# Performance work log

Measured on AMD Instinct MI355X. Metric: run time of the kernel, lower is better.

## Reference

```python
import jax, jax.numpy as jnp
import numpy as np

EMBED = 768
HEADS = 12
HEAD_DIM = EMBED // HEADS
NUM_BUCKETS = 32
MAX_DISTANCE = 128


def _relative_buckets(tgt_len, src_len):
    ctx = jnp.arange(tgt_len)[:, None]
    mem = jnp.arange(src_len)[None, :]
    rel = mem - ctx                                  # [T, S]
    nb = NUM_BUCKETS // 2                            # 16
    buckets = (rel > 0).astype(jnp.int32) * nb
    rp = jnp.abs(rel)
    max_exact = nb // 2                              # 8
    is_small = rp < max_exact
    rp_safe = jnp.maximum(rp, 1).astype(jnp.float32)
    large = max_exact + (
        jnp.log(rp_safe / max_exact) / np.log(MAX_DISTANCE / max_exact) * (nb - max_exact)
    ).astype(jnp.int32)
    large = jnp.minimum(large, nb - 1)
    buckets = buckets + jnp.where(is_small, rp, large)
    return buckets                                   # [T, S] int32


def setup_inputs() -> dict:
    key = jax.random.key(0)
    ks = jax.random.split(key, 12)
    T, B, E = 2048, 2, EMBED
    def xavier(k, shape, gain=1.0):
        fan_in, fan_out = shape[0], shape[1]
        a = gain * np.sqrt(6.0 / (fan_in + fan_out))
        return jax.random.uniform(k, shape, jnp.float32, -a, a)
    g = 1.0 / np.sqrt(2.0)
    return {
        "query": jax.random.normal(ks[0], (T, B, E), jnp.float32),
        "key": jax.random.normal(ks[1], (T, B, E), jnp.float32),
        "value": jax.random.normal(ks[2], (T, B, E), jnp.float32),
        "key_padding_mask": jnp.zeros((B, T), dtype=bool),
        # weights stored [in, out] (transpose of torch Linear)
        "Wq": xavier(ks[3], (E, E), g), "bq": jnp.zeros((E,), jnp.float32),
        "Wk": xavier(ks[4], (E, E), g), "bk": jnp.zeros((E,), jnp.float32),
        "Wv": xavier(ks[5], (E, E), g), "bv": jnp.zeros((E,), jnp.float32),
        "Wo": xavier(ks[6], (E, E), 1.0), "bo": jnp.zeros((E,), jnp.float32),
        "rel_bias": jax.random.normal(ks[7], (NUM_BUCKETS, HEADS), jnp.float32)
        * np.sqrt(2.0 / (NUM_BUCKETS + HEADS)),
    }


def reference(query, key, value, key_padding_mask, Wq, bq, Wk, bk, Wv, bv, Wo, bo, rel_bias):
    T, B, E = query.shape
    S = key.shape[0]
    scaling = HEAD_DIM ** -0.5
    q = (query @ Wq + bq) * scaling
    k = key @ Wk + bk
    v = value @ Wv + bv
    # [T,B,E] -> [B,H,T,D]
    def split_heads(x, L):
        return x.reshape(L, B, HEADS, HEAD_DIM).transpose(1, 2, 0, 3)
    qh, kh, vh = split_heads(q, T), split_heads(k, S), split_heads(v, S)
    # T5 relative position bias: [H, T, S]
    buckets = _relative_buckets(T, S)
    position_bias = rel_bias[buckets].transpose(2, 0, 1)  # [H,T,S]
    scores = jnp.einsum("bhtd,bhsd->bhts", qh, kh) + position_bias[None]
    scores = jnp.where(key_padding_mask[:, None, None, :], -jnp.inf, scores)
    probs = jax.nn.softmax(scores, axis=-1)
    attn = jnp.einsum("bhts,bhsd->bhtd", probs, vh)
    attn = attn.transpose(2, 0, 1, 3).reshape(T, B, E)
    return attn @ Wo + bo
```

## Files before the change

### kernel.cpp

```cpp
#include <hip/hip_runtime.h>
#include <hip/hip_bf16.h>

typedef __bf16 bf16;
typedef __bf16 bf16x8 __attribute__((ext_vector_type(8)));
typedef float f32x4 __attribute__((ext_vector_type(4)));

#define EMB 768
#define NH 12
#define HD 64
#define SEQ 2048
#define NBATCH 2
#define NREL (2 * SEQ - 1)
#define LOG2E 1.44269504088896f

__device__ __forceinline__ int swz(int bo) { return bo ^ ((bo >> 3) & 0x70); }
__device__ __forceinline__ int swz256(int bo) { return bo ^ ((bo >> 4) & 0x70); }
__device__ __forceinline__ int kpos(int s) {
  return (s & 0x23) | ((s & 0x04) << 2) | ((s & 0x18) >> 1);
}
__device__ __forceinline__ float fexp2(float x) {
  return __builtin_amdgcn_exp2f(x);
}

typedef __attribute__((address_space(3))) unsigned int lds_u32;
typedef __attribute__((address_space(1))) unsigned int glb_u32;
__device__ __forceinline__ void gld16(const void* g, void* l) {
  __builtin_amdgcn_global_load_lds((const glb_u32*)g, (lds_u32*)l, 16, 0, 0);
}

__global__ __launch_bounds__(256) void k_setup(
    const float* __restrict__ Xq, const float* __restrict__ Xk,
    const float* __restrict__ Xv, const float* __restrict__ Wq,
    const float* __restrict__ Wk, const float* __restrict__ Wv,
    const float* __restrict__ Wo, const unsigned char* __restrict__ mask,
    const float* __restrict__ rel_bias, bf16* __restrict__ ximg,
    bf16* __restrict__ wimg, float* __restrict__ bias_tab,
    unsigned long long* __restrict__ mbits) {
  __shared__ __align__(16) bf16 T[64 * 128];
  const int idx = blockIdx.x;
  const int tid = threadIdx.x;
  if (idx < 1152) {
    const int z = idx / 384, rem = idx % 384;
    const int mb = rem % 32, ks = rem / 32;
    const float* X = z == 0 ? Xq : z == 1 ? Xk : Xv;
    const int m0 = mb * 128, k0 = ks * 64;
    char* img = (char*)ximg + ((size_t)(z * 32 + mb) * 12 + ks) * 16384;
#pragma unroll
    for (int it = 0; it < 4; ++it) {
      int i = tid + it * 256;
      int mr = i >> 3, kc8 = (i & 7) * 8;
      const float* xp = X + (size_t)(m0 + mr) * EMB + k0 + kc8;
      float4 f0 = *(const float4*)xp, f1 = *(const float4*)(xp + 4);
      bf16x8 hh;
      hh[0] = (bf16)f0.x; hh[1] = (bf16)f0.y; hh[2] = (bf16)f0.z; hh[3] = (bf16)f0.w;
      hh[4] = (bf16)f1.x; hh[5] = (bf16)f1.y; hh[6] = (bf16)f1.z; hh[7] = (bf16)f1.w;
      *(bf16x8*)(img + swz(mr * 128 + kc8 * 2)) = hh;
    }
  } else if (idx < 1440) {
    const int i = idx - 1152;
    const int z = i / 72, rem = i % 72;
    const int nb = rem % 6, ks = rem / 6;
    const float* W = z == 0 ? Wq : z == 1 ? Wk : z == 2 ? Wv : Wo;
    const int n0 = nb * 128, k0 = ks * 64;
    {
      int kk = tid >> 2, nn0 = (tid & 3) * 32;
      const float* wp = W + (size_t)(k0 + kk) * EMB + n0 + nn0;
#pragma unroll
      for (int jq = 0; jq < 4; ++jq) {
        float4 f0 = *(const float4*)(wp + jq * 8);
        float4 f1 = *(const float4*)(wp + jq * 8 + 4);
        bf16x8 hh;
        hh[0] = (bf16)f0.x; hh[1] = (bf16)f0.y; hh[2] = (bf16)f0.z; hh[3] = (bf16)f0.w;
        hh[4] = (bf16)f1.x; hh[5] = (bf16)f1.y; hh[6] = (bf16)f1.z; hh[7] = (bf16)f1.w;
        *(bf16x8*)((char*)T + swz256(kk * 256 + (nn0 + jq * 8) * 2)) = hh;
      }
    }
    __syncthreads();
    {
      int nr = tid >> 1, kh = tid & 1;
      char* img = (char*)wimg + ((size_t)(z * 6 + nb) * 12 + ks) * 16384;
#pragma unroll
      for (int jq = 0; jq < 4; ++jq) {
        union { bf16 e[8]; uint4 u; } pk;
#pragma unroll
        for (int q = 0; q < 8; ++q)
          pk.e[q] = *(const bf16*)((char*)T + swz256((kh * 32 + jq * 8 + q) * 256 + nr * 2));
        *(uint4*)(img + swz(nr * 128 + (kh * 32 + jq * 8) * 2)) = pk.u;
      }
    }
  } else if (idx < 1456) {
    int i = (idx - 1440) * 256 + tid;
    if (i < NREL) {
      int rel = i - (SEQ - 1);
      int bkt = (rel > 0) ? 16 : 0;
      int rp = rel < 0 ? -rel : rel;
      if (rp < 8) {
        bkt += rp;
      } else {
        float lf = (logf((float)rp * 0.125f) / 2.7725887222397811f) * 8.0f;
        int large = 8 + (int)lf;
        bkt += (large < 15) ? large : 15;
      }
      for (int h = 0; h < NH; ++h)
        bias_tab[h * NREL + i] = rel_bias[bkt * NH + h] * LOG2E;
    }
  } else {
    int wid = (idx - 1456) * 4 + (tid >> 6);
    int lane = tid & 63;
    int b = wid >> 5, wd = wid & 31;
    unsigned long long m = __ballot(mask[b * SEQ + wd * 64 + lane] != 0);
    if (lane == 0) mbits[wid] = m;
  }
}

__global__ __launch_bounds__(256) void k_proj_qkv(
    const bf16* __restrict__ ximg, const bf16* __restrict__ wimg,
    const float* __restrict__ bq, const float* __restrict__ bk,
    const float* __restrict__ bv, bf16* __restrict__ oq,
    bf16* __restrict__ gk, bf16* __restrict__ gv) {
  __shared__ __align__(16) bf16 AB[2][2][8192];
  const int z = blockIdx.z;
  const float* bias = z == 0 ? bq : z == 1 ? bk : bv;
  const float scale = z == 0 ? 0.125f * LOG2E : 1.0f;
  const int mb = blockIdx.x, nb = blockIdx.y;
  const int m0 = mb * 128, n0 = nb * 128;
  const int tid = threadIdx.x, lane = tid & 63, w = tid >> 6;
  const int c = lane & 15, g = lane >> 4;
  const int mo = (w >> 1) * 64, no = (w & 1) * 64;
  const char* abase = (const char*)ximg + (size_t)(z * 32 + mb) * 12 * 16384;
  const char* bbase = (const char*)wimg + (size_t)(z * 6 + nb) * 12 * 16384;

#define PISSUE(KS, BUF) do {                                               \
    const char* a_ = abase + (size_t)(KS) * 16384;                         \
    const char* b_ = bbase + (size_t)(KS) * 16384;                         \
    _Pragma("unroll") for (int ch = 0; ch < 4; ++ch) {                     \
      int ck = w * 4 + ch;                                                 \
      gld16(a_ + ck * 1024 + lane * 16, (char*)AB[BUF][0] + ck * 1024);    \
      gld16(b_ + ck * 1024 + lane * 16, (char*)AB[BUF][1] + ck * 1024);    \
    }                                                                      \
  } while (0)

  PISSUE(0, 0);
  f32x4 acc[4][4] = {};
  asm volatile("s_waitcnt vmcnt(0)" ::: "memory");
  __syncthreads();
  for (int ks = 0; ks < 12; ++ks) {
    const int cur = ks & 1;
    if (ks < 11) PISSUE(ks + 1, cur ^ 1);
    const char* As = (const char*)AB[cur][0];
    const char* Bs = (const char*)AB[cur][1];
    __builtin_amdgcn_s_setprio(1);
#pragma unroll
    for (int kk = 0; kk < 2; ++kk) {
      bf16x8 av[4], bvf[4];
#pragma unroll
      for (int mf = 0; mf < 4; ++mf)
        av[mf] = *(const bf16x8*)(As + swz((mo + mf * 16 + c) * 128 + kk * 64 + g * 16));
#pragma unroll
      for (int nf = 0; nf < 4; ++nf)
        bvf[nf] = *(const bf16x8*)(Bs + swz((no + nf * 16 + c) * 128 + kk * 64 + g * 16));
#pragma unroll
      for (int mf = 0; mf < 4; ++mf)
#pragma unroll
        for (int nf = 0; nf < 4; ++nf)
          acc[mf][nf] = __builtin_amdgcn_mfma_f32_16x16x32_bf16(bvf[nf], av[mf], acc[mf][nf], 0, 0, 0);
    }
    __builtin_amdgcn_s_setprio(0);
    if (ks < 11) {
      asm volatile("s_waitcnt vmcnt(0)" ::: "memory");
      __syncthreads();
    }
  }
#pragma unroll
  for (int nf = 0; nf < 4; ++nf) {
    int n = n0 + no + nf * 16 + g * 4;
    float4 b4 = *(const float4*)&bias[n];
#pragma unroll
    for (int mf = 0; mf < 4; ++mf) {
      int m = m0 + mo + mf * 16 + c;
      float v0 = (acc[mf][nf][0] + b4.x) * scale;
      float v1 = (acc[mf][nf][1] + b4.y) * scale;
      float v2 = (acc[mf][nf][2] + b4.z) * scale;
      float v3 = (acc[mf][nf][3] + b4.w) * scale;
      if (z == 0) {
        union { bf16 e[4]; uint2 u; } pk;
        pk.e[0] = (bf16)v0; pk.e[1] = (bf16)v1; pk.e[2] = (bf16)v2; pk.e[3] = (bf16)v3;
        *(uint2*)(oq + (size_t)m * EMB + n) = pk.u;
      } else if (z == 1) {
        int t = m >> 1, bb = m & 1;
        int hh = n >> 6, d = n & 63;
        union { bf16 e[4]; uint2 u; } pk;
        pk.e[0] = (bf16)v0; pk.e[1] = (bf16)v1; pk.e[2] = (bf16)v2; pk.e[3] = (bf16)v3;
        char* base = (char*)gk + ((size_t)(bb * NH + hh) * 32 + (t >> 6)) * 8192;
        *(uint2*)(base + swz(kpos(t & 63) * 128 + (d & ~7) * 2) + (d & 4) * 2) = pk.u;
      } else {
        int s = m >> 1, bb = m & 1;
        int hh = n >> 6, d0 = n & 63;
        char* base = (char*)gv + ((size_t)(bb * NH + hh) * 32 + (s >> 6)) * 8192;
        int sc2 = (s & 63) * 2;
        *(bf16*)(base + (((d0 + 0) * 128 + sc2) ^ (((d0 + 0) & 7) << 4))) = (bf16)v0;
        *(bf16*)(base + (((d0 + 1) * 128 + sc2) ^ (((d0 + 1) & 7) << 4))) = (bf16)v1;
        *(bf16*)(base + (((d0 + 2) * 128 + sc2) ^ (((d0 + 2) & 7) << 4))) = (bf16)v2;
        *(bf16*)(base + (((d0 + 3) * 128 + sc2) ^ (((d0 + 3) & 7) << 4))) = (bf16)v3;
      }
    }
  }
#undef PISSUE
}

__global__ __launch_bounds__(256) void k_proj_out(
    const bf16* __restrict__ aimg, const bf16* __restrict__ wimg,
    const float* __restrict__ bias, float* __restrict__ out) {
  __shared__ __align__(16) bf16 AB[2][2][8192];
  const int mb = blockIdx.x, nb = blockIdx.y;
  const int m0 = mb * 128, n0 = nb * 128;
  const int tid = threadIdx.x, lane = tid & 63, w = tid >> 6;
  const int c = lane & 15, g = lane >> 4;
  const int mo = (w >> 1) * 64, no = (w & 1) * 64;
  const char* abase = (const char*)aimg + (size_t)mb * 12 * 16384;
  const char* bbase = (const char*)wimg + (size_t)(3 * 6 + nb) * 12 * 16384;

#define PISSUE(KS, BUF) do {                                               \
    const char* a_ = abase + (size_t)(KS) * 16384;                         \
    const char* b_ = bbase + (size_t)(KS) * 16384;                         \
    _Pragma("unroll") for (int ch = 0; ch < 4; ++ch) {                     \
      int ck = w * 4 + ch;                                                 \
      gld16(a_ + ck * 1024 + lane * 16, (char*)AB[BUF][0] + ck * 1024);    \
      gld16(b_ + ck * 1024 + lane * 16, (char*)AB[BUF][1] + ck * 1024);    \
    }                                                                      \
  } while (0)

  PISSUE(0, 0);
  f32x4 acc[4][4] = {};
  asm volatile("s_waitcnt vmcnt(0)" ::: "memory");
  __syncthreads();
  for (int ks = 0; ks < 12; ++ks) {
    const int cur = ks & 1;
    if (ks < 11) PISSUE(ks + 1, cur ^ 1);
    const char* As = (const char*)AB[cur][0];
    const char* Bs = (const char*)AB[cur][1];
    __builtin_amdgcn_s_setprio(1);
#pragma unroll
    for (int kk = 0; kk < 2; ++kk) {
      bf16x8 av[4], bvf[4];
#pragma unroll
      for (int mf = 0; mf < 4; ++mf)
        av[mf] = *(const bf16x8*)(As + swz((mo + mf * 16 + c) * 128 + kk * 64 + g * 16));
#pragma unroll
      for (int nf = 0; nf < 4; ++nf)
        bvf[nf] = *(const bf16x8*)(Bs + swz((no + nf * 16 + c) * 128 + kk * 64 + g * 16));
#pragma unroll
      for (int mf = 0; mf < 4; ++mf)
#pragma unroll
        for (int nf = 0; nf < 4; ++nf)
          acc[mf][nf] = __builtin_amdgcn_mfma_f32_16x16x32_bf16(bvf[nf], av[mf], acc[mf][nf], 0, 0, 0);
    }
    __builtin_amdgcn_s_setprio(0);
    if (ks < 11) {
      asm volatile("s_waitcnt vmcnt(0)" ::: "memory");
      __syncthreads();
    }
  }
#pragma unroll
  for (int nf = 0; nf < 4; ++nf) {
    int n = n0 + no + nf * 16 + g * 4;
    float4 b4 = *(const float4*)&bias[n];
#pragma unroll
    for (int mf = 0; mf < 4; ++mf) {
      int m = m0 + mo + mf * 16 + c;
      float4 v;
      v.x = acc[mf][nf][0] + b4.x;
      v.y = acc[mf][nf][1] + b4.y;
      v.z = acc[mf][nf][2] + b4.z;
      v.w = acc[mf][nf][3] + b4.w;
      *(float4*)(out + (size_t)m * EMB + n) = v;
    }
  }
#undef PISSUE
}

__global__ __launch_bounds__(256, 4) void k_attn(
    const bf16* __restrict__ qb, const bf16* __restrict__ gk,
    const bf16* __restrict__ gv, const unsigned long long* __restrict__ mbits,
    const float* __restrict__ bias_tab, bf16* __restrict__ aimg) {
  __shared__ __align__(16) bf16 KV[2][2][4096];
  __shared__ float Bslow[384];
  const int bh = blockIdx.x;
  const int b = bh / NH, h = bh % NH;
  const int t0 = blockIdx.y * 64;
  const int tid = threadIdx.x;
  const int lane = tid & 63, w = tid >> 6;
  const int c = lane & 15, g = lane >> 4;
  const float NEGINF = -__builtin_inff();
  const int tl = w * 16 + c;

  const char* kimg = (const char*)gk + (size_t)bh * 32 * 8192;
  const char* vimg = (const char*)gv + (size_t)bh * 32 * 8192;

#define ISSUE(IT, BUF) do {                                                  \
    const char* ks_ = kimg + (size_t)(IT) * 8192;                            \
    const char* vs_ = vimg + (size_t)(IT) * 8192;                            \
    _Pragma("unroll") for (int jj = 0; jj < 2; ++jj) {                       \
      int ch = w * 2 + jj;                                                   \
      gld16(ks_ + ch * 1024 + lane * 16, (char*)KV[BUF][0] + ch * 1024);     \
      gld16(vs_ + ch * 1024 + lane * 16, (char*)KV[BUF][1] + ch * 1024);     \
    }                                                                        \
  } while (0)

  ISSUE(0, 0);
  bf16x8 qf[2];
  {
    const bf16* qp = qb + (size_t)((t0 + tl) * NBATCH + b) * EMB + h * 64 + g * 8;
    qf[0] = *(const bf16x8*)qp;
    qf[1] = *(const bf16x8*)(qp + 32);
  }
  const float* btab = bias_tab + h * NREL + (SEQ - 1);
  for (int j = tid; j < 384; j += 256) Bslow[j] = btab[j - 192];
  const float cpos = btab[SEQ - 1];
  const float cneg = btab[-(SEQ - 1)];

  bf16x8 ones8;
#pragma unroll
  for (int j = 0; j < 8; ++j) ones8[j] = (bf16)1.0f;

  float m_p = -1e30f;
  f32x4 lacc = {0.f, 0.f, 0.f, 0.f};
  f32x4 o[4] = {};

  asm volatile("s_waitcnt vmcnt(0)" ::: "memory");
  __syncthreads();

  for (int it = 0; it < 32; ++it) {
    const int cur = it & 1;
    if (it < 31) ISSUE(it + 1, cur ^ 1);
    const unsigned long long mb = mbits[b * 32 + it];
    const char* Ks = (const char*)KV[cur][0];
    const char* Vs = (const char*)KV[cur][1];

    f32x4 sacc[4] = {};
    __builtin_amdgcn_s_setprio(1);
#pragma unroll
    for (int kk = 0; kk < 2; ++kk) {
#pragma unroll
      for (int nf = 0; nf < 4; ++nf) {
        bf16x8 kf = *(const bf16x8*)(Ks + swz((nf * 16 + c) * 128 + kk * 64 + g * 16));
        sacc[nf] = __builtin_amdgcn_mfma_f32_16x16x32_bf16(kf, qf[kk], sacc[nf], 0, 0, 0);
      }
    }
    __builtin_amdgcn_s_setprio(0);

    const int s0 = it * 64;
    const int d = s0 - t0;
    const bool slow = (d > -192) && (d < 192);
    const float cb = slow ? 0.f : (d >= 192 ? cpos : cneg);

    if (slow) {
      const int bidx = d - tl + 192;
#pragma unroll
      for (int nf = 0; nf < 4; ++nf) {
        int sb = 32 * (nf >> 1) + g * 8 + (nf & 1) * 4;
#pragma unroll
        for (int r = 0; r < 4; ++r) sacc[nf][r] += Bslow[bidx + sb + r];
      }
    }
    if (mb) {
#pragma unroll
      for (int nf = 0; nf < 4; ++nf) {
        int sb = 32 * (nf >> 1) + g * 8 + (nf & 1) * 4;
#pragma unroll
        for (int r = 0; r < 4; ++r)
          if ((mb >> (sb + r)) & 1) sacc[nf][r] = NEGINF;
      }
    }
    f32x4 mx;
#pragma unroll
    for (int r = 0; r < 4; ++r)
      mx[r] = fmaxf(fmaxf(sacc[0][r], sacc[1][r]), fmaxf(sacc[2][r], sacc[3][r]));
    float rmax = fmaxf(fmaxf(mx[0], mx[1]), fmaxf(mx[2], mx[3]));
    rmax = fmaxf(rmax, __shfl_xor(rmax, 16, 64));
    rmax = fmaxf(rmax, __shfl_xor(rmax, 32, 64));
    const float rm = rmax + cb;

    if (!__all(rm <= m_p + 11.5f)) {
      float m_new = fmaxf(m_p, rm);
      float scl = fexp2(m_p - m_new);
      m_p = m_new;
#pragma unroll
      for (int r = 0; r < 4; ++r) {
        float so = __shfl(scl, g * 4 + r, 64);
        lacc[r] *= so;
#pragma unroll
        for (int nf2 = 0; nf2 < 4; ++nf2) o[nf2][r] *= so;
      }
    }
    const float msh = m_p - cb;
    bf16x8 pa[2];
#pragma unroll
    for (int kk = 0; kk < 2; ++kk)
#pragma unroll
      for (int j = 0; j < 8; ++j)
        pa[kk][j] = (bf16)fexp2(sacc[2 * kk + (j >> 2)][j & 3] - msh);

    __builtin_amdgcn_s_setprio(1);
    lacc = __builtin_amdgcn_mfma_f32_16x16x32_bf16(pa[0], ones8, lacc, 0, 0, 0);
    lacc = __builtin_amdgcn_mfma_f32_16x16x32_bf16(pa[1], ones8, lacc, 0, 0, 0);
#pragma unroll
    for (int kk = 0; kk < 2; ++kk) {
#pragma unroll
      for (int nf2 = 0; nf2 < 4; ++nf2) {
        bf16x8 vbf = *(const bf16x8*)(Vs + swz((nf2 * 16 + c) * 128 + kk * 64 + g * 16));
        o[nf2] = __builtin_amdgcn_mfma_f32_16x16x32_bf16(pa[kk], vbf, o[nf2], 0, 0, 0);
      }
    }
    __builtin_amdgcn_s_setprio(0);

    if (it < 31) {
      asm volatile("s_waitcnt vmcnt(0)" ::: "memory");
      __syncthreads();
    }
  }
#pragma unroll
  for (int r = 0; r < 4; ++r) {
    float inv = 1.0f / lacc[r];
    int t = t0 + w * 16 + g * 4 + r;
    int m = t * NBATCH + b;
    char* base = (char*)aimg + ((size_t)(m >> 7) * 12 + h) * 16384;
    int mr128 = (m & 127) * 128;
#pragma unroll
    for (int nf2 = 0; nf2 < 4; ++nf2) {
      int dd = nf2 * 16 + c;
      *(bf16*)(base + swz(mr128 + dd * 2)) = (bf16)(o[nf2][r] * inv);
    }
  }
#undef ISSUE
}

extern "C" void kernel_launch(void* const* d_in, const int* in_sizes, int n_in,
                              void* d_out, int out_size, void* d_ws, size_t ws_size,
                              hipStream_t stream) {
  const float* query = (const float*)d_in[0];
  const float* key_ = (const float*)d_in[1];
  const float* value = (const float*)d_in[2];
  const unsigned char* kpm = (const unsigned char*)d_in[3];
  const float* Wq = (const float*)d_in[4];
  const float* bq = (const float*)d_in[5];
  const float* Wk = (const float*)d_in[6];
  const float* bk = (const float*)d_in[7];
  const float* Wv = (const float*)d_in[8];
  const float* bv = (const float*)d_in[9];
  const float* Wo = (const float*)d_in[10];
  const float* bo = (const float*)d_in[11];
  const float* rel_bias = (const float*)d_in[12];
  float* out = (float*)d_out;

  char* ws = (char*)d_ws;
  const size_t SZb = (size_t)SEQ * NBATCH * EMB * sizeof(bf16);
  const size_t WIMG = (size_t)4 * 6 * 12 * 16384;
  bf16* qbb = (bf16*)(ws);
  bf16* gkb = (bf16*)(ws + SZb);
  bf16* gvb = (bf16*)(ws + 2 * SZb);
  bf16* wimg = (bf16*)(ws + 3 * SZb);
  float* bias_tab = (float*)(ws + 3 * SZb + WIMG);
  unsigned long long* mbits =
      (unsigned long long*)(ws + 3 * SZb + WIMG + 196608);
  bf16* ximg = (bf16*)(ws + 3 * SZb + WIMG + 196608 + 512);
  bf16* aimg = ximg;

  k_setup<<<1472, 256, 0, stream>>>(query, key_, value, Wq, Wk, Wv, Wo,
                                    kpm, rel_bias, ximg, wimg, bias_tab, mbits);
  k_proj_qkv<<<dim3(32, 6, 3), 256, 0, stream>>>(
      ximg, wimg, bq, bk, bv, qbb, gkb, gvb);
  k_attn<<<dim3(NBATCH * NH, SEQ / 64), 256, 0, stream>>>(
      qbb, gkb, gvb, mbits, bias_tab, aimg);
  k_proj_out<<<dim3(32, 6), 256, 0, stream>>>(aimg, wimg, bo, out);
}
```

Baseline: 94.32 us.

## Switch attention to 32x32x16 MFMA with split-KV waves and LDS merge

Rewrites the attention inner loop to use 32x32x16 bf16 MFMAs. Each pair of waves shares 32 query rows and splits the 64-key tile between them, with a final LDS-based merge of max, sum and partial outputs. The row sum is now accumulated in VALU instead of through ones-vector MFMAs, and P is re-laid out with permlane32 swaps for the PV MFMA. The K layout permutation in setup is dropped to match the new access pattern. This adds an epilogue merge with extra syncs and LDS traffic.

Result: slower. 114.8 us (+21.7%).

```diff
diff --git a/kernel.cpp b/kernel.cpp
--- a/kernel.cpp
+++ b/kernel.cpp
@@ -4,6 +4,7 @@
 typedef __bf16 bf16;
 typedef __bf16 bf16x8 __attribute__((ext_vector_type(8)));
 typedef float f32x4 __attribute__((ext_vector_type(4)));
+typedef float f32x16 __attribute__((ext_vector_type(16)));
 
 #define EMB 768
 #define NH 12
@@ -15,9 +16,6 @@
 
 __device__ __forceinline__ int swz(int bo) { return bo ^ ((bo >> 3) & 0x70); }
 __device__ __forceinline__ int swz256(int bo) { return bo ^ ((bo >> 4) & 0x70); }
-__device__ __forceinline__ int kpos(int s) {
-  return (s & 0x23) | ((s & 0x04) << 2) | ((s & 0x18) >> 1);
-}
 __device__ __forceinline__ float fexp2(float x) {
   return __builtin_amdgcn_exp2f(x);
 }
@@ -192,7 +190,7 @@
         union { bf16 e[4]; uint2 u; } pk;
         pk.e[0] = (bf16)v0; pk.e[1] = (bf16)v1; pk.e[2] = (bf16)v2; pk.e[3] = (bf16)v3;
         char* base = (char*)gk + ((size_t)(bb * NH + hh) * 32 + (t >> 6)) * 8192;
-        *(uint2*)(base + swz(kpos(t & 63) * 128 + (d & ~7) * 2) + (d & 4) * 2) = pk.u;
+        *(uint2*)(base + swz((t & 63) * 128 + (d & ~7) * 2) + (d & 4) * 2) = pk.u;
       } else {
         int s = m >> 1, bb = m & 1;
         int hh = n >> 6, d0 = n & 63;
@@ -290,9 +288,10 @@
   const int t0 = blockIdx.y * 64;
   const int tid = threadIdx.x;
   const int lane = tid & 63, w = tid >> 6;
-  const int c = lane & 15, g = lane >> 4;
+  const int tg = w >> 1, sh = w & 1;
+  const int lr = lane & 31, hi = lane >> 5;
+  const int tl = tg * 32 + lr;
   const float NEGINF = -__builtin_inff();
-  const int tl = w * 16 + c;
 
   const char* kimg = (const char*)gk + (size_t)bh * 32 * 8192;
   const char* vimg = (const char*)gv + (size_t)bh * 32 * 8192;
@@ -308,24 +307,19 @@
   } while (0)
 
   ISSUE(0, 0);
-  bf16x8 qf[2];
+  bf16x8 qf[4];
   {
-    const bf16* qp = qb + (size_t)((t0 + tl) * NBATCH + b) * EMB + h * 64 + g * 8;
-    qf[0] = *(const bf16x8*)qp;
-    qf[1] = *(const bf16x8*)(qp + 32);
+    const bf16* qp = qb + (size_t)((t0 + tl) * NBATCH + b) * EMB + h * 64 + 8 * hi;
+#pragma unroll
+    for (int kk = 0; kk < 4; ++kk) qf[kk] = *(const bf16x8*)(qp + kk * 16);
   }
   const float* btab = bias_tab + h * NREL + (SEQ - 1);
   for (int j = tid; j < 384; j += 256) Bslow[j] = btab[j - 192];
   const float cpos = btab[SEQ - 1];
   const float cneg = btab[-(SEQ - 1)];
 
-  bf16x8 ones8;
-#pragma unroll
-  for (int j = 0; j < 8; ++j) ones8[j] = (bf16)1.0f;
-
-  float m_p = -1e30f;
-  f32x4 lacc = {0.f, 0.f, 0.f, 0.f};
-  f32x4 o[4] = {};
+  float m_p = -1e30f, l_p = 0.f;
+  f32x16 o0 = {}, o1 = {};
 
   asm volatile("s_waitcnt vmcnt(0)" ::: "memory");
   __syncthreads();
@@ -337,15 +331,12 @@
     const char* Ks = (const char*)KV[cur][0];
     const char* Vs = (const char*)KV[cur][1];
 
-    f32x4 sacc[4] = {};
+    f32x16 sacc = {};
     __builtin_amdgcn_s_setprio(1);
 #pragma unroll
-    for (int kk = 0; kk < 2; ++kk) {
-#pragma unroll
-      for (int nf = 0; nf < 4; ++nf) {
-        bf16x8 kf = *(const bf16x8*)(Ks + swz((nf * 16 + c) * 128 + kk * 64 + g * 16));
-        sacc[nf] = __builtin_amdgcn_mfma_f32_16x16x32_bf16(kf, qf[kk], sacc[nf], 0, 0, 0);
-      }
+    for (int kk = 0; kk < 4; ++kk) {
+      bf16x8 kf = *(const bf16x8*)(Ks + swz((sh * 32 + lr) * 128 + (kk * 16 + 8 * hi) * 2));
+      sacc = __builtin_amdgcn_mfma_f32_32x32x16_bf16(kf, qf[kk], sacc, 0, 0, 0);
     }
     __builtin_amdgcn_s_setprio(0);
 
@@ -355,29 +346,23 @@
     const float cb = slow ? 0.f : (d >= 192 ? cpos : cneg);
 
     if (slow) {
-      const int bidx = d - tl + 192;
-#pragma unroll
-      for (int nf = 0; nf < 4; ++nf) {
-        int sb = 32 * (nf >> 1) + g * 8 + (nf & 1) * 4;
-#pragma unroll
-        for (int r = 0; r < 4; ++r) sacc[nf][r] += Bslow[bidx + sb + r];
+      const int bidx0 = d + sh * 32 + 4 * hi - tl + 192;
+#pragma unroll
+      for (int reg = 0; reg < 16; ++reg)
+        sacc[reg] += Bslow[bidx0 + (reg & 3) + 8 * (reg >> 2)];
+    }
+    if (mb) {
+#pragma unroll
+      for (int reg = 0; reg < 16; ++reg) {
+        int sbit = sh * 32 + (reg & 3) + 8 * (reg >> 2) + 4 * hi;
+        if ((mb >> sbit) & 1) sacc[reg] = NEGINF;
       }
     }
-    if (mb) {
-#pragma unroll
-      for (int nf = 0; nf < 4; ++nf) {
-        int sb = 32 * (nf >> 1) + g * 8 + (nf & 1) * 4;
-#pragma unroll
-        for (int r = 0; r < 4; ++r)
-          if ((mb >> (sb + r)) & 1) sacc[nf][r] = NEGINF;
-      }
-    }
-    f32x4 mx;
+    f32x4 t4;
 #pragma unroll
     for (int r = 0; r < 4; ++r)
-      mx[r] = fmaxf(fmaxf(sacc[0][r], sacc[1][r]), fmaxf(sacc[2][r], sacc[3][r]));
-    float rmax = fmaxf(fmaxf(mx[0], mx[1]), fmaxf(mx[2], mx[3]));
-    rmax = fmaxf(rmax, __shfl_xor(rmax, 16, 64));
+      t4[r] = fmaxf(fmaxf(sacc[r], sacc[4 + r]), fmaxf(sacc[8 + r], sacc[12 + r]));
+    float rmax = fmaxf(fmaxf(t4[0], t4[1]), fmaxf(t4[2], t4[3]));
     rmax = fmaxf(rmax, __shfl_xor(rmax, 32, 64));
     const float rm = rmax + cb;
 
@@ -385,32 +370,41 @@
       float m_new = fmaxf(m_p, rm);
       float scl = fexp2(m_p - m_new);
       m_p = m_new;
-#pragma unroll
-      for (int r = 0; r < 4; ++r) {
-        float so = __shfl(scl, g * 4 + r, 64);
-        lacc[r] *= so;
-#pragma unroll
-        for (int nf2 = 0; nf2 < 4; ++nf2) o[nf2][r] *= so;
-      }
+      l_p *= scl;
+#pragma unroll
+      for (int i = 0; i < 16; ++i) { o0[i] *= scl; o1[i] *= scl; }
     }
     const float msh = m_p - cb;
-    bf16x8 pa[2];
-#pragma unroll
-    for (int kk = 0; kk < 2; ++kk)
-#pragma unroll
-      for (int j = 0; j < 8; ++j)
-        pa[kk][j] = (bf16)fexp2(sacc[2 * kk + (j >> 2)][j & 3] - msh);
+    union { bf16 e[16]; unsigned u[8]; } pkv;
+    f32x4 rs = {0.f, 0.f, 0.f, 0.f};
+#pragma unroll
+    for (int reg = 0; reg < 16; ++reg) {
+      float e = fexp2(sacc[reg] - msh);
+      rs[reg & 3] += e;
+      pkv.e[reg] = (bf16)e;
+    }
+    float rsum = (rs[0] + rs[1]) + (rs[2] + rs[3]);
+    rsum += __shfl_xor(rsum, 32, 64);
+    l_p += rsum;
+
+    unsigned a0 = pkv.u[0], a1 = pkv.u[1], b0 = pkv.u[2], b1 = pkv.u[3];
+    unsigned c0 = pkv.u[4], c1 = pkv.u[5], e0 = pkv.u[6], e1 = pkv.u[7];
+    asm volatile("v_permlane32_swap_b32 %0, %1" : "+v"(a0), "+v"(b0));
+    asm volatile("v_permlane32_swap_b32 %0, %1" : "+v"(a1), "+v"(b1));
+    asm volatile("v_permlane32_swap_b32 %0, %1" : "+v"(c0), "+v"(e0));
+    asm volatile("v_permlane32_swap_b32 %0, %1" : "+v"(c1), "+v"(e1));
+    union { unsigned u[4]; bf16x8 v; } B0, B1;
+    B0.u[0] = a0; B0.u[1] = a1; B0.u[2] = b0; B0.u[3] = b1;
+    B1.u[0] = c0; B1.u[1] = c1; B1.u[2] = e0; B1.u[3] = e1;
 
     __builtin_amdgcn_s_setprio(1);
-    lacc = __builtin_amdgcn_mfma_f32_16x16x32_bf16(pa[0], ones8, lacc, 0, 0, 0);
-    lacc = __builtin_amdgcn_mfma_f32_16x16x32_bf16(pa[1], ones8, lacc, 0, 0, 0);
 #pragma unroll
     for (int kk = 0; kk < 2; ++kk) {
-#pragma unroll
-      for (int nf2 = 0; nf2 < 4; ++nf2) {
-        bf16x8 vbf = *(const bf16x8*)(Vs + swz((nf2 * 16 + c) * 128 + kk * 64 + g * 16));
-        o[nf2] = __builtin_amdgcn_mfma_f32_16x16x32_bf16(pa[kk], vbf, o[nf2], 0, 0, 0);
-      }
+      bf16x8 vf0 = *(const bf16x8*)(Vs + swz((0 * 32 + lr) * 128 + (sh * 32 + kk * 16 + 8 * hi) * 2));
+      bf16x8 vf1 = *(const bf16x8*)(Vs + swz((1 * 32 + lr) * 128 + (sh * 32 + kk * 16 + 8 * hi) * 2));
+      bf16x8 pB = kk ? B1.v : B0.v;
+      o0 = __builtin_amdgcn_mfma_f32_32x32x16_bf16(vf0, pB, o0, 0, 0, 0);
+      o1 = __builtin_amdgcn_mfma_f32_32x32x16_bf16(vf1, pB, o1, 0, 0, 0);
     }
     __builtin_amdgcn_s_setprio(0);
 
@@ -419,17 +413,42 @@
       __syncthreads();
     }
   }
-#pragma unroll
-  for (int r = 0; r < 4; ++r) {
-    float inv = 1.0f / lacc[r];
-    int t = t0 + w * 16 + g * 4 + r;
+  __syncthreads();
+  float* mlb = (float*)KV;
+  float* ob = mlb + 256;
+  if (hi == 0) {
+    mlb[(tg * 2 + sh) * 64 + lr] = m_p;
+    mlb[(tg * 2 + sh) * 64 + 32 + lr] = l_p;
+  }
+  __syncthreads();
+  const int base_own = (tg * 2 + sh) * 64, base_oth = (tg * 2 + (sh ^ 1)) * 64;
+  float ms = mlb[base_own + lr], ls = mlb[base_own + 32 + lr];
+  float mo2 = mlb[base_oth + lr], lo2 = mlb[base_oth + 32 + lr];
+  float M = fmaxf(ms, mo2);
+  float a = fexp2(ms - M);
+  float lt = ls * a + lo2 * fexp2(mo2 - M);
+  if (sh == 1) {
+#pragma unroll
+    for (int reg = 0; reg < 16; ++reg) {
+      int dd = (reg & 3) + 8 * (reg >> 2) + 4 * hi;
+      ob[tg * 2048 + dd * 32 + lr] = o0[reg] * a;
+      ob[tg * 2048 + (dd + 32) * 32 + lr] = o1[reg] * a;
+    }
+  }
+  __syncthreads();
+  if (sh == 0) {
+    float inv = 1.0f / lt;
+    int t = t0 + tl;
     int m = t * NBATCH + b;
     char* base = (char*)aimg + ((size_t)(m >> 7) * 12 + h) * 16384;
     int mr128 = (m & 127) * 128;
 #pragma unroll
-    for (int nf2 = 0; nf2 < 4; ++nf2) {
-      int dd = nf2 * 16 + c;
-      *(bf16*)(base + swz(mr128 + dd * 2)) = (bf16)(o[nf2][r] * inv);
+    for (int reg = 0; reg < 16; ++reg) {
+      int dd = (reg & 3) + 8 * (reg >> 2) + 4 * hi;
+      float v0 = (o0[reg] * a + ob[tg * 2048 + dd * 32 + lr]) * inv;
+      float v1 = (o1[reg] * a + ob[tg * 2048 + (dd + 32) * 32 + lr]) * inv;
+      *(bf16*)(base + swz(mr128 + dd * 2)) = (bf16)v0;
+      *(bf16*)(base + swz(mr128 + (dd + 32) * 2)) = (bf16)v1;
     }
   }
 #undef ISSUE
```
